# Optimization experiments

Measured on AMD Instinct MI355X. Metric: run time of the kernel, lower is better.

## Reference

```python
import jax, jax.numpy as jnp
import numpy as np

H = 768   # hidden_dim * SMPL_NR_JOINTS = 32 * 24
O = 72    # output_dim * SMPL_NR_JOINTS = 3 * 24
B = 256
T = 100   # max_len (tgt.size(1))
SRC_LEN = 16


def setup_inputs() -> dict:
    key = jax.random.key(0)
    ks = jax.random.split(key, 10)
    s = 1.0 / np.sqrt(H)
    return {
        "src": jax.random.normal(ks[0], (B, SRC_LEN, H), jnp.float32),
        "tgt": jax.random.normal(ks[1], (B, T, O), jnp.float32),
        "h0": jax.random.normal(ks[2], (B, H), jnp.float32),
        "c0": jax.random.normal(ks[3], (B, H), jnp.float32),
        "W_ih": jax.random.uniform(ks[4], (4 * H, H), jnp.float32, -s, s),
        "W_hh": jax.random.uniform(ks[5], (4 * H, H), jnp.float32, -s, s),
        "b_ih": jax.random.uniform(ks[6], (4 * H,), jnp.float32, -s, s),
        "b_hh": jax.random.uniform(ks[7], (4 * H,), jnp.float32, -s, s),
        "W_post": jax.random.uniform(ks[8], (O, H), jnp.float32, -s, s),
        "b_post": jax.random.uniform(ks[9], (O,), jnp.float32, -s, s),
    }


def reference(src, tgt, h0, c0, W_ih, W_hh, b_ih, b_hh, W_post, b_post):
    max_len = tgt.shape[1]
    bias = b_ih + b_hh  # [4H]

    def step(carry, _):
        x, h, c = carry  # each [B, H]
        gates = x @ W_ih.T + h @ W_hh.T + bias  # [B, 4H]
        i, f, g, o = jnp.split(gates, 4, axis=-1)  # PyTorch gate order i,f,g,o
        c = jax.nn.sigmoid(f) * c + jax.nn.sigmoid(i) * jnp.tanh(g)
        h = jax.nn.sigmoid(o) * jnp.tanh(c)
        return (h, h, c), h  # decoder output feeds back as next input

    x0 = src[:, -1]  # out = src[:, -1].unsqueeze(1)
    _, outs = jax.lax.scan(step, (x0, h0, c0), None, length=max_len)  # [T, B, H]
    outs = jnp.transpose(outs, (1, 0, 2))  # [B, T, H]
    return outs @ W_post.T + b_post  # [B, T, O]
```

## Files before the change

### kernel.cpp

```cpp
#include <hip/hip_runtime.h>
#include <hip/hip_bf16.h>
#include <math.h>

#define H 768
#define B 256
#define T 100

typedef __attribute__((ext_vector_type(8))) short short8;
typedef __attribute__((ext_vector_type(4))) float f32x4;
typedef unsigned long long u64;

static __device__ __forceinline__ float sigm(float x) {
    return 1.0f / (1.0f + __expf(-x));
}
static __device__ __forceinline__ float tanh_fast(float x) {
    return 1.0f - 2.0f / (__expf(2.0f * x) + 1.0f);
}

__global__ void prep_all(const float* __restrict__ src, const float* __restrict__ h0,
                         const float* __restrict__ Wih, const float* __restrict__ Whh,
                         const float* __restrict__ bih, const float* __restrict__ bhh,
                         const float* __restrict__ Wpost,
                         __hip_bfloat16* __restrict__ Wc,
                         __hip_bfloat16* __restrict__ Wcat,
                         float* __restrict__ bias,
                         __hip_bfloat16* __restrict__ Wp,
                         __hip_bfloat16* __restrict__ A0,
                         u64* __restrict__ sig64)
{
    const int bx = blockIdx.x;
    const int y  = blockIdx.y;
    const int k  = bx * 256 + threadIdx.x;
    if (y < 3072) {
        float a = Wih[y * H + k];
        float b = Whh[y * H + k];
        Wc[y * H + k] = __float2bfloat16(a + b);
        Wcat[y * 1536 + k] = __float2bfloat16(a);
        Wcat[y * 1536 + H + k] = __float2bfloat16(b);
        if (bx == 0 && threadIdx.x == 0) bias[y] = bih[y] + bhh[y];
    } else if (y < 3152) {
        int r = y - 3072;
        Wp[r * H + k] = (r < 72) ? __float2bfloat16(Wpost[r * H + k])
                                 : __float2bfloat16(0.0f);
    } else if (y < 3408) {
        int b = y - 3152;
        A0[b * 1536 + k] = __float2bfloat16(src[(b * 16 + 15) * H + k]);
        A0[b * 1536 + H + k] = __float2bfloat16(h0[b * H + k]);
    } else {
        sig64[(size_t)(y - 3408) * 768 + k] = 0ull;
    }
}

#define LDS_H_STRIDE  772
#define LDS_T0_STRIDE 1540
#define XCH_STRIDE    17

#define LDW8(n0,n1,n2,n3,n4,n5,n6,n7, p) \
    asm volatile("global_load_dwordx4 %0, %8, off\n\t" \
                 "global_load_dwordx4 %1, %8, off offset:64\n\t" \
                 "global_load_dwordx4 %2, %8, off offset:128\n\t" \
                 "global_load_dwordx4 %3, %8, off offset:192\n\t" \
                 "global_load_dwordx4 %4, %8, off offset:256\n\t" \
                 "global_load_dwordx4 %5, %8, off offset:320\n\t" \
                 "global_load_dwordx4 %6, %8, off offset:384\n\t" \
                 "global_load_dwordx4 %7, %8, off offset:448\n\t" \
                 "s_waitcnt vmcnt(0)" \
                 : "=&v"(n0),"=&v"(n1),"=&v"(n2),"=&v"(n3), \
                   "=&v"(n4),"=&v"(n5),"=&v"(n6),"=&v"(n7) \
                 : "v"(p))

#define KSTEP(nm, idx) { \
    short8 a_ = *(const short8*)(&lds_h[col * LDS_H_STRIDE + (idx) * 32 + quad * 8]); \
    acc = __builtin_amdgcn_mfma_f32_16x16x32_bf16(a_, nm, acc, 0, 0, 0); }

static __device__ __forceinline__ bool sig_ok(u64 x) {
    return (unsigned short)x && (unsigned short)(x >> 16) &&
           (unsigned short)(x >> 32) && (unsigned short)(x >> 48);
}

__global__ __launch_bounds__(768, 3) void lstm_persist(
    const __hip_bfloat16* __restrict__ Wc,
    const __hip_bfloat16* __restrict__ Wcat,
    const float* __restrict__ bias,
    const float* __restrict__ c0in,
    const __hip_bfloat16* __restrict__ A0,
    unsigned* sig)
{
    const int mtg  = blockIdx.x >> 4;
    const int jg   = blockIdx.x & 15;
    const int tid  = threadIdx.x;
    const int lane = tid & 63;
    const int wave = tid >> 6;
    const int col  = lane & 15;
    const int quad = lane >> 4;
    const int jt_l = wave >> 2;
    const int gate = wave & 3;
    const int j    = jg * 48 + jt_l * 16 + col;

    __shared__ short lds_h[16 * LDS_T0_STRIDE];
    __shared__ float xch[12 * 16 * XCH_STRIDE];

    const short* wptr = (const short*)Wc + (size_t)(gate * H + j) * H + quad * 8;
    short8 w00,w01,w02,w03,w04,w05,w06,w07,w08,w09,w10,w11,
           w12,w13,w14,w15,w16,w17,w18,w19,w20,w21,w22,w23;
    LDW8(w00,w01,w02,w03,w04,w05,w06,w07, wptr);
    LDW8(w08,w09,w10,w11,w12,w13,w14,w15, wptr + 256);
    LDW8(w16,w17,w18,w19,w20,w21,w22,w23, wptr + 512);

    const int p    = tid;
    const int bb   = p / 24;
    const int jp   = p % 24;
    const int jloc = jp * 2;
    const int cjt  = jloc >> 4;
    const int jcol = jloc & 15;
    const int bglob = mtg * 16 + bb;
    const int jglob = jg * 48 + jloc;
    float c0v = 0.f, c1v = 0.f;
    float bi0=0,bi1=0,bf0=0,bf1=0,bg0=0,bg1=0,bo0=0,bo1=0;
    if (p < 384) {
        c0v = c0in[(size_t)bglob * H + jglob];
        c1v = c0in[(size_t)bglob * H + jglob + 1];
        bi0 = bias[0*H + jglob]; bi1 = bias[0*H + jglob + 1];
        bf0 = bias[1*H + jglob]; bf1 = bias[1*H + jglob + 1];
        bg0 = bias[2*H + jglob]; bg1 = bias[2*H + jglob + 1];
        bo0 = bias[3*H + jglob]; bo1 = bias[3*H + jglob + 1];
    }

    const u64* sig64c = (const u64*)sig;
    const int r0  = tid / 192;
    const int wrd = tid % 192;

    for (int t = 0; t < T; ++t) {
        f32x4 acc = {0.f, 0.f, 0.f, 0.f};

        if (t == 0) {
            const u64* a8 = (const u64*)((const short*)A0 + (size_t)(mtg * 16) * 1536);
#pragma unroll
            for (int i = 0; i < 8; ++i) {
                int idx = tid + i * 768;
                int br  = idx / 384;
                int ch  = idx % 384;
                *(u64*)&lds_h[br * LDS_T0_STRIDE + ch * 4] = a8[(size_t)br * 384 + ch];
            }
            __syncthreads();

            const short* wq = (const short*)Wcat + (size_t)(gate * H + j) * 1536 + quad * 8;
            for (int kk = 0; kk < 48; ++kk) {
                short8 a_ = *(const short8*)(&lds_h[col * LDS_T0_STRIDE + kk * 32 + quad * 8]);
                short8 b_ = *(const short8*)(wq + kk * 32);
                acc = __builtin_amdgcn_mfma_f32_16x16x32_bf16(a_, b_, acc, 0, 0, 0);
            }
        } else {
            const u64* hb = sig64c + ((size_t)(t - 1) * B + (size_t)(mtg * 16)) * 192 + wrd;
            u64 x0 = __hip_atomic_load(hb + (size_t)(r0     ) * 192,
                                       __ATOMIC_RELAXED, __HIP_MEMORY_SCOPE_AGENT);
            u64 x1 = __hip_atomic_load(hb + (size_t)(r0 +  4) * 192,
                                       __ATOMIC_RELAXED, __HIP_MEMORY_SCOPE_AGENT);
            u64 x2 = __hip_atomic_load(hb + (size_t)(r0 +  8) * 192,
                                       __ATOMIC_RELAXED, __HIP_MEMORY_SCOPE_AGENT);
            u64 x3 = __hip_atomic_load(hb + (size_t)(r0 + 12) * 192,
                                       __ATOMIC_RELAXED, __HIP_MEMORY_SCOPE_AGENT);
            unsigned pending = 0xFu;
            if (sig_ok(x0)) { *(u64*)&lds_h[(r0     ) * LDS_H_STRIDE + wrd * 4] = ~x0; pending &= ~1u; }
            if (sig_ok(x1)) { *(u64*)&lds_h[(r0 +  4) * LDS_H_STRIDE + wrd * 4] = ~x1; pending &= ~2u; }
            if (sig_ok(x2)) { *(u64*)&lds_h[(r0 +  8) * LDS_H_STRIDE + wrd * 4] = ~x2; pending &= ~4u; }
            if (sig_ok(x3)) { *(u64*)&lds_h[(r0 + 12) * LDS_H_STRIDE + wrd * 4] = ~x3; pending &= ~8u; }
            int guard = 0;
            while (pending && ++guard < (1 << 22)) {
                __builtin_amdgcn_s_sleep(4);
                if (pending & 1u) x0 = __hip_atomic_load(hb + (size_t)(r0     ) * 192,
                                        __ATOMIC_RELAXED, __HIP_MEMORY_SCOPE_AGENT);
                if (pending & 2u) x1 = __hip_atomic_load(hb + (size_t)(r0 +  4) * 192,
                                        __ATOMIC_RELAXED, __HIP_MEMORY_SCOPE_AGENT);
                if (pending & 4u) x2 = __hip_atomic_load(hb + (size_t)(r0 +  8) * 192,
                                        __ATOMIC_RELAXED, __HIP_MEMORY_SCOPE_AGENT);
                if (pending & 8u) x3 = __hip_atomic_load(hb + (size_t)(r0 + 12) * 192,
                                        __ATOMIC_RELAXED, __HIP_MEMORY_SCOPE_AGENT);
                if ((pending & 1u) && sig_ok(x0)) { *(u64*)&lds_h[(r0     ) * LDS_H_STRIDE + wrd * 4] = ~x0; pending &= ~1u; }
                if ((pending & 2u) && sig_ok(x1)) { *(u64*)&lds_h[(r0 +  4) * LDS_H_STRIDE + wrd * 4] = ~x1; pending &= ~2u; }
                if ((pending & 4u) && sig_ok(x2)) { *(u64*)&lds_h[(r0 +  8) * LDS_H_STRIDE + wrd * 4] = ~x2; pending &= ~4u; }
                if ((pending & 8u) && sig_ok(x3)) { *(u64*)&lds_h[(r0 + 12) * LDS_H_STRIDE + wrd * 4] = ~x3; pending &= ~8u; }
            }
            __syncthreads();

            KSTEP(w00,0)  KSTEP(w01,1)  KSTEP(w02,2)  KSTEP(w03,3)
            KSTEP(w04,4)  KSTEP(w05,5)  KSTEP(w06,6)  KSTEP(w07,7)
            KSTEP(w08,8)  KSTEP(w09,9)  KSTEP(w10,10) KSTEP(w11,11)
            KSTEP(w12,12) KSTEP(w13,13) KSTEP(w14,14) KSTEP(w15,15)
            KSTEP(w16,16) KSTEP(w17,17) KSTEP(w18,18) KSTEP(w19,19)
            KSTEP(w20,20) KSTEP(w21,21) KSTEP(w22,22) KSTEP(w23,23)
        }

        float* xw = &xch[(size_t)wave * 16 * XCH_STRIDE];
#pragma unroll
        for (int r = 0; r < 4; ++r)
            xw[(quad * 4 + r) * XCH_STRIDE + col] = acc[r];
        __syncthreads();

        if (p < 384) {
            const float* xg = &xch[(size_t)(cjt * 4) * 16 * XCH_STRIDE + bb * XCH_STRIDE + jcol];
            const int gs = 16 * XCH_STRIDE;
            float i0 = xg[0*gs] + bi0, i1 = xg[0*gs + 1] + bi1;
            float f0 = xg[1*gs] + bf0, f1 = xg[1*gs + 1] + bf1;
            float g0 = xg[2*gs] + bg0, g1 = xg[2*gs + 1] + bg1;
            float o0 = xg[3*gs] + bo0, o1 = xg[3*gs + 1] + bo1;
            float cn0 = sigm(f0) * c0v + sigm(i0) * tanh_fast(g0);
            float cn1 = sigm(f1) * c1v + sigm(i1) * tanh_fast(g1);
            c0v = cn0; c1v = cn1;
            __hip_bfloat16 h0b = __float2bfloat16(sigm(o0) * tanh_fast(cn0));
            __hip_bfloat16 h1b = __float2bfloat16(sigm(o1) * tanh_fast(cn1));
            unsigned lo = (unsigned)(unsigned short)~(*(unsigned short*)&h0b);
            unsigned hi = (unsigned)(unsigned short)~(*(unsigned short*)&h1b);
            __hip_atomic_store(&sig[((size_t)t * B + bglob) * 384 + (jglob >> 1)],
                               lo | (hi << 16),
                               __ATOMIC_RELAXED, __HIP_MEMORY_SCOPE_AGENT);
        }
        __syncthreads();
    }
}

__global__ __launch_bounds__(64) void proj(
    const short* __restrict__ Hs,
    const __hip_bfloat16* __restrict__ Wp,
    const float* __restrict__ bpost,
    float* __restrict__ out)
{
    const int mt = blockIdx.x;
    const int lane = threadIdx.x;
    const int col = lane & 15;
    const int quad = lane >> 4;

    const short* Ap = Hs + (size_t)(mt * 16 + col) * H + quad * 8;
    const short* Wb = (const short*)Wp;

    f32x4 acc[5];
#pragma unroll
    for (int nt = 0; nt < 5; ++nt) acc[nt] = (f32x4){0.f, 0.f, 0.f, 0.f};

    for (int k = 0; k < H; k += 32) {
        short8 a = ~(*(const short8*)(Ap + k));
#pragma unroll
        for (int nt = 0; nt < 5; ++nt) {
            short8 b = *(const short8*)(Wb + (size_t)(nt * 16 + col) * H + quad * 8 + k);
            acc[nt] = __builtin_amdgcn_mfma_f32_16x16x32_bf16(a, b, acc[nt], 0, 0, 0);
        }
    }

#pragma unroll
    for (int nt = 0; nt < 5; ++nt) {
        const int o = nt * 16 + col;
        if (o < 72) {
            const float bb = bpost[o];
#pragma unroll
            for (int r = 0; r < 4; ++r) {
                const int m = mt * 16 + quad * 4 + r;
                const int t = m >> 8;
                const int b = m & 255;
                out[((size_t)b * T + t) * 72 + o] = acc[nt][r] + bb;
            }
        }
    }
}


extern "C" void kernel_launch(void* const* d_in, const int* in_sizes, int n_in,
                              void* d_out, int out_size, void* d_ws, size_t ws_size,
                              hipStream_t stream) {
    const float* src   = (const float*)d_in[0];
    const float* h0    = (const float*)d_in[2];
    const float* c0    = (const float*)d_in[3];
    const float* Wih   = (const float*)d_in[4];
    const float* Whh   = (const float*)d_in[5];
    const float* bih   = (const float*)d_in[6];
    const float* bhh   = (const float*)d_in[7];
    const float* Wpost = (const float*)d_in[8];
    const float* bpost = (const float*)d_in[9];
    float* out = (float*)d_out;

    char* ws = (char*)d_ws;
    __hip_bfloat16* Wcat = (__hip_bfloat16*)(ws + 0);
    __hip_bfloat16* Wc   = (__hip_bfloat16*)(ws + 9437184);
    float*          bias = (float*)(ws + 14155776);
    __hip_bfloat16* Wp   = (__hip_bfloat16*)(ws + 14168064);
    __hip_bfloat16* A0   = (__hip_bfloat16*)(ws + 14290944);
    unsigned*       sig  = (unsigned*)(ws + 15863808);

    prep_all<<<dim3(3, 9808), 256, 0, stream>>>(src, h0, Wih, Whh, bih, bhh, Wpost,
                                                Wc, Wcat, bias, Wp, A0, (u64*)sig);

    lstm_persist<<<256, 768, 0, stream>>>(Wc, Wcat, bias, c0, A0, sig);

    proj<<<1600, 64, 0, stream>>>((const short*)sig, Wp, bpost, out);
}
```

Baseline: 460.5 us.

## Remap persistent LSTM blocks by XCD and poll with non-coherent sc0 loads

At kernel start each block reads its hardware XCD id and takes a slot from a per-XCD counter. When every XCD holds exactly 32 blocks, it remaps (batch tile, hidden group) so each batch tile's 16 hidden groups sit on one XCD, keeping h-state exchange inside a shared L2. The h-state polling now first uses sc0 loads with shorter sleeps and falls back to agent-scope atomic loads after a few sweeps. This is meant to cut cross-XCD coherence latency in the per-timestep handoff. It adds a startup grid-wide barrier, and it relies on all 256 blocks being co-resident and on sc0 loads observing other blocks' writes within the same XCD.

```diff
diff --git a/kernel.cpp b/kernel.cpp
--- a/kernel.cpp
+++ b/kernel.cpp
@@ -26,7 +26,8 @@
                          float* __restrict__ bias,
                          __hip_bfloat16* __restrict__ Wp,
                          __hip_bfloat16* __restrict__ A0,
-                         u64* __restrict__ sig64)
+                         u64* __restrict__ sig64,
+                         unsigned* __restrict__ ctrl)
 {
     const int bx = blockIdx.x;
     const int y  = blockIdx.y;
@@ -48,12 +49,15 @@
         A0[b * 1536 + H + k] = __float2bfloat16(h0[b * H + k]);
     } else {
         sig64[(size_t)(y - 3408) * 768 + k] = 0ull;
+        if (y == 3408 && bx == 0 && threadIdx.x < 16) ctrl[threadIdx.x] = 0u;
     }
 }
 
 #define LDS_H_STRIDE  772
 #define LDS_T0_STRIDE 1540
 #define XCH_STRIDE    17
+#define GUARD_MAX     (1 << 22)
+#define ESC_SWEEPS    4
 
 #define LDW8(n0,n1,n2,n3,n4,n5,n6,n7, p) \
     asm volatile("global_load_dwordx4 %0, %8, off\n\t" \
@@ -69,6 +73,24 @@
                    "=&v"(n4),"=&v"(n5),"=&v"(n6),"=&v"(n7) \
                  : "v"(p))
 
+#define LDP4_SC0(x0,x1,x2,x3, p0,p1,p2,p3) \
+    asm volatile("global_load_dwordx2 %0, %4, off sc0\n\t" \
+                 "global_load_dwordx2 %1, %5, off sc0\n\t" \
+                 "global_load_dwordx2 %2, %6, off sc0\n\t" \
+                 "global_load_dwordx2 %3, %7, off sc0\n\t" \
+                 "s_waitcnt vmcnt(0)" \
+                 : "=&v"(x0),"=&v"(x1),"=&v"(x2),"=&v"(x3) \
+                 : "v"(p0),"v"(p1),"v"(p2),"v"(p3))
+
+#define AG_LD(p) __hip_atomic_load((p), __ATOMIC_RELAXED, __HIP_MEMORY_SCOPE_AGENT)
+
+static __device__ __forceinline__ u64 ld2_sc0(const u64* p) {
+    u64 r;
+    asm volatile("global_load_dwordx2 %0, %1, off sc0\n\ts_waitcnt vmcnt(0)"
+                 : "=v"(r) : "v"(p));
+    return r;
+}
+
 #define KSTEP(nm, idx) { \
     short8 a_ = *(const short8*)(&lds_h[col * LDS_H_STRIDE + (idx) * 32 + quad * 8]); \
     acc = __builtin_amdgcn_mfma_f32_16x16x32_bf16(a_, nm, acc, 0, 0, 0); }
@@ -84,10 +106,9 @@
     const float* __restrict__ bias,
     const float* __restrict__ c0in,
     const __hip_bfloat16* __restrict__ A0,
-    unsigned* sig)
+    unsigned* sig,
+    unsigned* ctrl)
 {
-    const int mtg  = blockIdx.x >> 4;
-    const int jg   = blockIdx.x & 15;
     const int tid  = threadIdx.x;
     const int lane = tid & 63;
     const int wave = tid >> 6;
@@ -95,10 +116,39 @@
     const int quad = lane >> 4;
     const int jt_l = wave >> 2;
     const int gate = wave & 3;
-    const int j    = jg * 48 + jt_l * 16 + col;
 
     __shared__ short lds_h[16 * LDS_T0_STRIDE];
     __shared__ float xch[12 * 16 * XCH_STRIDE];
+    __shared__ unsigned s_role[2];
+
+    if (tid == 0) {
+        unsigned xcd;
+        asm volatile("s_getreg_b32 %0, hwreg(HW_REG_XCC_ID)" : "=s"(xcd));
+        xcd &= 7u;
+        unsigned slot = __hip_atomic_fetch_add(&ctrl[xcd], 1u,
+                            __ATOMIC_RELAXED, __HIP_MEMORY_SCOPE_AGENT);
+        if (slot >= 32u)
+            __hip_atomic_store(&ctrl[9], 1u, __ATOMIC_RELEASE, __HIP_MEMORY_SCOPE_AGENT);
+        __hip_atomic_fetch_add(&ctrl[8], 1u, __ATOMIC_RELEASE, __HIP_MEMORY_SCOPE_AGENT);
+        int cg = 0;
+        while (__hip_atomic_load(&ctrl[8], __ATOMIC_ACQUIRE, __HIP_MEMORY_SCOPE_AGENT) < 256u
+               && ++cg < GUARD_MAX)
+            __builtin_amdgcn_s_sleep(8);
+        s_role[0] = xcd * 32u + slot;
+        s_role[1] = __hip_atomic_load(&ctrl[9], __ATOMIC_ACQUIRE, __HIP_MEMORY_SCOPE_AGENT);
+    }
+    __syncthreads();
+    const bool LOCAL = (s_role[1] == 0u);
+    int mtg, jg;
+    if (LOCAL) {
+        const unsigned slot32 = s_role[0] & 31u;
+        mtg = (int)((s_role[0] >> 5) * 2u + (slot32 >> 4));
+        jg  = (int)(slot32 & 15u);
+    } else {
+        mtg = blockIdx.x >> 4;
+        jg  = blockIdx.x & 15;
+    }
+    const int j = jg * 48 + jt_l * 16 + col;
 
     const short* wptr = (const short*)Wc + (size_t)(gate * H + j) * H + quad * 8;
     short8 w00,w01,w02,w03,w04,w05,w06,w07,w08,w09,w10,w11,
@@ -152,34 +202,30 @@
             }
         } else {
             const u64* hb = sig64c + ((size_t)(t - 1) * B + (size_t)(mtg * 16)) * 192 + wrd;
-            u64 x0 = __hip_atomic_load(hb + (size_t)(r0     ) * 192,
-                                       __ATOMIC_RELAXED, __HIP_MEMORY_SCOPE_AGENT);
-            u64 x1 = __hip_atomic_load(hb + (size_t)(r0 +  4) * 192,
-                                       __ATOMIC_RELAXED, __HIP_MEMORY_SCOPE_AGENT);
-            u64 x2 = __hip_atomic_load(hb + (size_t)(r0 +  8) * 192,
-                                       __ATOMIC_RELAXED, __HIP_MEMORY_SCOPE_AGENT);
-            u64 x3 = __hip_atomic_load(hb + (size_t)(r0 + 12) * 192,
-                                       __ATOMIC_RELAXED, __HIP_MEMORY_SCOPE_AGENT);
+            const u64* q0 = hb + (size_t)(r0     ) * 192;
+            const u64* q1 = hb + (size_t)(r0 +  4) * 192;
+            const u64* q2 = hb + (size_t)(r0 +  8) * 192;
+            const u64* q3 = hb + (size_t)(r0 + 12) * 192;
+            u64 x0, x1, x2, x3;
+            LDP4_SC0(x0, x1, x2, x3, q0, q1, q2, q3);
             unsigned pending = 0xFu;
             if (sig_ok(x0)) { *(u64*)&lds_h[(r0     ) * LDS_H_STRIDE + wrd * 4] = ~x0; pending &= ~1u; }
             if (sig_ok(x1)) { *(u64*)&lds_h[(r0 +  4) * LDS_H_STRIDE + wrd * 4] = ~x1; pending &= ~2u; }
             if (sig_ok(x2)) { *(u64*)&lds_h[(r0 +  8) * LDS_H_STRIDE + wrd * 4] = ~x2; pending &= ~4u; }
             if (sig_ok(x3)) { *(u64*)&lds_h[(r0 + 12) * LDS_H_STRIDE + wrd * 4] = ~x3; pending &= ~8u; }
             int guard = 0;
-            while (pending && ++guard < (1 << 22)) {
-                __builtin_amdgcn_s_sleep(4);
-                if (pending & 1u) x0 = __hip_atomic_load(hb + (size_t)(r0     ) * 192,
-                                        __ATOMIC_RELAXED, __HIP_MEMORY_SCOPE_AGENT);
-                if (pending & 2u) x1 = __hip_atomic_load(hb + (size_t)(r0 +  4) * 192,
-                                        __ATOMIC_RELAXED, __HIP_MEMORY_SCOPE_AGENT);
-                if (pending & 4u) x2 = __hip_atomic_load(hb + (size_t)(r0 +  8) * 192,
-                                        __ATOMIC_RELAXED, __HIP_MEMORY_SCOPE_AGENT);
-                if (pending & 8u) x3 = __hip_atomic_load(hb + (size_t)(r0 + 12) * 192,
-                                        __ATOMIC_RELAXED, __HIP_MEMORY_SCOPE_AGENT);
-                if ((pending & 1u) && sig_ok(x0)) { *(u64*)&lds_h[(r0     ) * LDS_H_STRIDE + wrd * 4] = ~x0; pending &= ~1u; }
-                if ((pending & 2u) && sig_ok(x1)) { *(u64*)&lds_h[(r0 +  4) * LDS_H_STRIDE + wrd * 4] = ~x1; pending &= ~2u; }
-                if ((pending & 4u) && sig_ok(x2)) { *(u64*)&lds_h[(r0 +  8) * LDS_H_STRIDE + wrd * 4] = ~x2; pending &= ~4u; }
-                if ((pending & 8u) && sig_ok(x3)) { *(u64*)&lds_h[(r0 + 12) * LDS_H_STRIDE + wrd * 4] = ~x3; pending &= ~8u; }
+            while (pending && ++guard < GUARD_MAX) {
+                if (guard < ESC_SWEEPS) __builtin_amdgcn_s_sleep(2);
+                else                    __builtin_amdgcn_s_sleep(4);
+                const bool esc = (guard >= ESC_SWEEPS);
+                if (pending & 1u) { x0 = esc ? AG_LD(q0) : ld2_sc0(q0);
+                    if (sig_ok(x0)) { *(u64*)&lds_h[(r0     ) * LDS_H_STRIDE + wrd * 4] = ~x0; pending &= ~1u; } }
+                if (pending & 2u) { x1 = esc ? AG_LD(q1) : ld2_sc0(q1);
+                    if (sig_ok(x1)) { *(u64*)&lds_h[(r0 +  4) * LDS_H_STRIDE + wrd * 4] = ~x1; pending &= ~2u; } }
+                if (pending & 4u) { x2 = esc ? AG_LD(q2) : ld2_sc0(q2);
+                    if (sig_ok(x2)) { *(u64*)&lds_h[(r0 +  8) * LDS_H_STRIDE + wrd * 4] = ~x2; pending &= ~4u; } }
+                if (pending & 8u) { x3 = esc ? AG_LD(q3) : ld2_sc0(q3);
+                    if (sig_ok(x3)) { *(u64*)&lds_h[(r0 + 12) * LDS_H_STRIDE + wrd * 4] = ~x3; pending &= ~8u; } }
             }
             __syncthreads();
 
@@ -283,12 +329,13 @@
     float*          bias = (float*)(ws + 14155776);
     __hip_bfloat16* Wp   = (__hip_bfloat16*)(ws + 14168064);
     __hip_bfloat16* A0   = (__hip_bfloat16*)(ws + 14290944);
+    unsigned*       ctrl = (unsigned*)(ws + 15077376);
     unsigned*       sig  = (unsigned*)(ws + 15863808);
 
     prep_all<<<dim3(3, 9808), 256, 0, stream>>>(src, h0, Wih, Whh, bih, bhh, Wpost,
-                                                Wc, Wcat, bias, Wp, A0, (u64*)sig);
-
-    lstm_persist<<<256, 768, 0, stream>>>(Wc, Wcat, bias, c0, A0, sig);
+                                                Wc, Wcat, bias, Wp, A0, (u64*)sig, ctrl);
+
+    lstm_persist<<<256, 768, 0, stream>>>(Wc, Wcat, bias, c0, A0, sig, ctrl);
 
     proj<<<1600, 64, 0, stream>>>((const short*)sig, Wp, bpost, out);
 }
```

After: 737.0 us. 1.6x slower.

## Add per-block step counters to gate polling before reading hidden-state signals

Applied to the files above, without the earlier changes.

Adds a per-block flag array that each block bumps with a release store after finishing a timestep. Before loading the previous step's hidden state, 16 threads spin on the 16 producer flags for their batch group, then all threads read the data once with sc1 vector loads. This replaces all 768 threads repeatedly polling the self-validating payload words, aiming to cut memory traffic and contention during the cross-block exchange. The cost is an extra flag round trip, a block barrier and a full vmcnt wait on every step, which could add latency on the critical path.

```diff
diff --git a/kernel.cpp b/kernel.cpp
--- a/kernel.cpp
+++ b/kernel.cpp
@@ -26,7 +26,8 @@
                          float* __restrict__ bias,
                          __hip_bfloat16* __restrict__ Wp,
                          __hip_bfloat16* __restrict__ A0,
-                         u64* __restrict__ sig64)
+                         u64* __restrict__ sig64,
+                         unsigned* __restrict__ flags)
 {
     const int bx = blockIdx.x;
     const int y  = blockIdx.y;
@@ -48,12 +49,14 @@
         A0[b * 1536 + H + k] = __float2bfloat16(h0[b * H + k]);
     } else {
         sig64[(size_t)(y - 3408) * 768 + k] = 0ull;
+        if (y == 3408 && bx == 0) flags[threadIdx.x] = 0u;
     }
 }
 
 #define LDS_H_STRIDE  772
 #define LDS_T0_STRIDE 1540
 #define XCH_STRIDE    17
+#define GUARD_MAX     (1 << 22)
 
 #define LDW8(n0,n1,n2,n3,n4,n5,n6,n7, p) \
     asm volatile("global_load_dwordx4 %0, %8, off\n\t" \
@@ -69,6 +72,17 @@
                    "=&v"(n4),"=&v"(n5),"=&v"(n6),"=&v"(n7) \
                  : "v"(p))
 
+#define LDP4_AG(x0,x1,x2,x3, p0,p1,p2,p3) \
+    asm volatile("global_load_dwordx2 %0, %4, off sc1\n\t" \
+                 "global_load_dwordx2 %1, %5, off sc1\n\t" \
+                 "global_load_dwordx2 %2, %6, off sc1\n\t" \
+                 "global_load_dwordx2 %3, %7, off sc1\n\t" \
+                 "s_waitcnt vmcnt(0)" \
+                 : "=&v"(x0),"=&v"(x1),"=&v"(x2),"=&v"(x3) \
+                 : "v"(p0),"v"(p1),"v"(p2),"v"(p3))
+
+#define AG_LD(p) __hip_atomic_load((p), __ATOMIC_RELAXED, __HIP_MEMORY_SCOPE_AGENT)
+
 #define KSTEP(nm, idx) { \
     short8 a_ = *(const short8*)(&lds_h[col * LDS_H_STRIDE + (idx) * 32 + quad * 8]); \
     acc = __builtin_amdgcn_mfma_f32_16x16x32_bf16(a_, nm, acc, 0, 0, 0); }
@@ -84,7 +98,8 @@
     const float* __restrict__ bias,
     const float* __restrict__ c0in,
     const __hip_bfloat16* __restrict__ A0,
-    unsigned* sig)
+    unsigned* sig,
+    unsigned* flags)
 {
     const int mtg  = blockIdx.x >> 4;
     const int jg   = blockIdx.x & 15;
@@ -151,35 +166,40 @@
                 acc = __builtin_amdgcn_mfma_f32_16x16x32_bf16(a_, b_, acc, 0, 0, 0);
             }
         } else {
+            if (tid < 16) {
+                const unsigned tgt = (unsigned)t;
+                unsigned v = AG_LD(&flags[mtg * 16 + tid]);
+                int fg = 0;
+                while (v < tgt && ++fg < GUARD_MAX) {
+                    __builtin_amdgcn_s_sleep(1);
+                    v = AG_LD(&flags[mtg * 16 + tid]);
+                }
+            }
+            __syncthreads();
+
             const u64* hb = sig64c + ((size_t)(t - 1) * B + (size_t)(mtg * 16)) * 192 + wrd;
-            u64 x0 = __hip_atomic_load(hb + (size_t)(r0     ) * 192,
-                                       __ATOMIC_RELAXED, __HIP_MEMORY_SCOPE_AGENT);
-            u64 x1 = __hip_atomic_load(hb + (size_t)(r0 +  4) * 192,
-                                       __ATOMIC_RELAXED, __HIP_MEMORY_SCOPE_AGENT);
-            u64 x2 = __hip_atomic_load(hb + (size_t)(r0 +  8) * 192,
-                                       __ATOMIC_RELAXED, __HIP_MEMORY_SCOPE_AGENT);
-            u64 x3 = __hip_atomic_load(hb + (size_t)(r0 + 12) * 192,
-                                       __ATOMIC_RELAXED, __HIP_MEMORY_SCOPE_AGENT);
+            const u64* q0 = hb + (size_t)(r0     ) * 192;
+            const u64* q1 = hb + (size_t)(r0 +  4) * 192;
+            const u64* q2 = hb + (size_t)(r0 +  8) * 192;
+            const u64* q3 = hb + (size_t)(r0 + 12) * 192;
+            u64 x0, x1, x2, x3;
+            LDP4_AG(x0, x1, x2, x3, q0, q1, q2, q3);
             unsigned pending = 0xFu;
             if (sig_ok(x0)) { *(u64*)&lds_h[(r0     ) * LDS_H_STRIDE + wrd * 4] = ~x0; pending &= ~1u; }
             if (sig_ok(x1)) { *(u64*)&lds_h[(r0 +  4) * LDS_H_STRIDE + wrd * 4] = ~x1; pending &= ~2u; }
             if (sig_ok(x2)) { *(u64*)&lds_h[(r0 +  8) * LDS_H_STRIDE + wrd * 4] = ~x2; pending &= ~4u; }
             if (sig_ok(x3)) { *(u64*)&lds_h[(r0 + 12) * LDS_H_STRIDE + wrd * 4] = ~x3; pending &= ~8u; }
             int guard = 0;
-            while (pending && ++guard < (1 << 22)) {
+            while (pending && ++guard < GUARD_MAX) {
                 __builtin_amdgcn_s_sleep(4);
-                if (pending & 1u) x0 = __hip_atomic_load(hb + (size_t)(r0     ) * 192,
-                                        __ATOMIC_RELAXED, __HIP_MEMORY_SCOPE_AGENT);
-                if (pending & 2u) x1 = __hip_atomic_load(hb + (size_t)(r0 +  4) * 192,
-                                        __ATOMIC_RELAXED, __HIP_MEMORY_SCOPE_AGENT);
-                if (pending & 4u) x2 = __hip_atomic_load(hb + (size_t)(r0 +  8) * 192,
-                                        __ATOMIC_RELAXED, __HIP_MEMORY_SCOPE_AGENT);
-                if (pending & 8u) x3 = __hip_atomic_load(hb + (size_t)(r0 + 12) * 192,
-                                        __ATOMIC_RELAXED, __HIP_MEMORY_SCOPE_AGENT);
-                if ((pending & 1u) && sig_ok(x0)) { *(u64*)&lds_h[(r0     ) * LDS_H_STRIDE + wrd * 4] = ~x0; pending &= ~1u; }
-                if ((pending & 2u) && sig_ok(x1)) { *(u64*)&lds_h[(r0 +  4) * LDS_H_STRIDE + wrd * 4] = ~x1; pending &= ~2u; }
-                if ((pending & 4u) && sig_ok(x2)) { *(u64*)&lds_h[(r0 +  8) * LDS_H_STRIDE + wrd * 4] = ~x2; pending &= ~4u; }
-                if ((pending & 8u) && sig_ok(x3)) { *(u64*)&lds_h[(r0 + 12) * LDS_H_STRIDE + wrd * 4] = ~x3; pending &= ~8u; }
+                if (pending & 1u) { x0 = AG_LD(q0);
+                    if (sig_ok(x0)) { *(u64*)&lds_h[(r0     ) * LDS_H_STRIDE + wrd * 4] = ~x0; pending &= ~1u; } }
+                if (pending & 2u) { x1 = AG_LD(q1);
+                    if (sig_ok(x1)) { *(u64*)&lds_h[(r0 +  4) * LDS_H_STRIDE + wrd * 4] = ~x1; pending &= ~2u; } }
+                if (pending & 4u) { x2 = AG_LD(q2);
+                    if (sig_ok(x2)) { *(u64*)&lds_h[(r0 +  8) * LDS_H_STRIDE + wrd * 4] = ~x2; pending &= ~4u; } }
+                if (pending & 8u) { x3 = AG_LD(q3);
+                    if (sig_ok(x3)) { *(u64*)&lds_h[(r0 + 12) * LDS_H_STRIDE + wrd * 4] = ~x3; pending &= ~8u; } }
             }
             __syncthreads();
 
@@ -215,7 +235,12 @@
                                lo | (hi << 16),
                                __ATOMIC_RELAXED, __HIP_MEMORY_SCOPE_AGENT);
         }
+        asm volatile("s_waitcnt vmcnt(0)" ::: "memory");
         __syncthreads();
+
+        if (tid == 0)
+            __hip_atomic_store(&flags[mtg * 16 + jg], (unsigned)(t + 1),
+                               __ATOMIC_RELEASE, __HIP_MEMORY_SCOPE_AGENT);
     }
 }
 
@@ -283,12 +308,13 @@
     float*          bias = (float*)(ws + 14155776);
     __hip_bfloat16* Wp   = (__hip_bfloat16*)(ws + 14168064);
     __hip_bfloat16* A0   = (__hip_bfloat16*)(ws + 14290944);
+    unsigned*       flags= (unsigned*)(ws + 15077376);
     unsigned*       sig  = (unsigned*)(ws + 15863808);
 
     prep_all<<<dim3(3, 9808), 256, 0, stream>>>(src, h0, Wih, Whh, bih, bhh, Wpost,
-                                                Wc, Wcat, bias, Wp, A0, (u64*)sig);
-
-    lstm_persist<<<256, 768, 0, stream>>>(Wc, Wcat, bias, c0, A0, sig);
+                                                Wc, Wcat, bias, Wp, A0, (u64*)sig, flags);
+
+    lstm_persist<<<256, 768, 0, stream>>>(Wc, Wcat, bias, c0, A0, sig, flags);
 
     proj<<<1600, 64, 0, stream>>>((const short*)sig, Wp, bpost, out);
 }
```

Result: slower. 899.9 us (+95.4%).

## Fuse output projection into persistent LSTM kernel tail

Applied to the files above, without the earlier changes.

Removes the separate projection kernel and computes the output projection at the end of the persistent LSTM kernel. Each wave handles one timestep for its batch tile, reading stored h from the signal buffer with sc1 loads, and the final timestep is first waited for and staged into LDS. This saves a kernel launch and lets the projection run on blocks already resident. In exchange the projection uses only 100 waves per batch group, with uneven load across blocks, and it relies on the spin-wait for the last step's h.

```diff
diff --git a/kernel.cpp b/kernel.cpp
--- a/kernel.cpp
+++ b/kernel.cpp
@@ -69,6 +69,17 @@
                    "=&v"(n4),"=&v"(n5),"=&v"(n6),"=&v"(n7) \
                  : "v"(p))
 
+#define LDA6(n0,n1,n2,n3,n4,n5, p) \
+    asm volatile("global_load_dwordx4 %0, %6, off sc1\n\t" \
+                 "global_load_dwordx4 %1, %6, off offset:64 sc1\n\t" \
+                 "global_load_dwordx4 %2, %6, off offset:128 sc1\n\t" \
+                 "global_load_dwordx4 %3, %6, off offset:192 sc1\n\t" \
+                 "global_load_dwordx4 %4, %6, off offset:256 sc1\n\t" \
+                 "global_load_dwordx4 %5, %6, off offset:320 sc1\n\t" \
+                 "s_waitcnt vmcnt(0)" \
+                 : "=&v"(n0),"=&v"(n1),"=&v"(n2),"=&v"(n3),"=&v"(n4),"=&v"(n5) \
+                 : "v"(p))
+
 #define KSTEP(nm, idx) { \
     short8 a_ = *(const short8*)(&lds_h[col * LDS_H_STRIDE + (idx) * 32 + quad * 8]); \
     acc = __builtin_amdgcn_mfma_f32_16x16x32_bf16(a_, nm, acc, 0, 0, 0); }
@@ -84,7 +95,10 @@
     const float* __restrict__ bias,
     const float* __restrict__ c0in,
     const __hip_bfloat16* __restrict__ A0,
-    unsigned* sig)
+    unsigned* sig,
+    const __hip_bfloat16* __restrict__ Wp,
+    const float* __restrict__ bpost,
+    float* __restrict__ out)
 {
     const int mtg  = blockIdx.x >> 4;
     const int jg   = blockIdx.x & 15;
@@ -217,46 +231,90 @@
         }
         __syncthreads();
     }
-}
-
-__global__ __launch_bounds__(64) void proj(
-    const short* __restrict__ Hs,
-    const __hip_bfloat16* __restrict__ Wp,
-    const float* __restrict__ bpost,
-    float* __restrict__ out)
-{
-    const int mt = blockIdx.x;
-    const int lane = threadIdx.x;
-    const int col = lane & 15;
-    const int quad = lane >> 4;
-
-    const short* Ap = Hs + (size_t)(mt * 16 + col) * H + quad * 8;
-    const short* Wb = (const short*)Wp;
-
-    f32x4 acc[5];
-#pragma unroll
-    for (int nt = 0; nt < 5; ++nt) acc[nt] = (f32x4){0.f, 0.f, 0.f, 0.f};
-
-    for (int k = 0; k < H; k += 32) {
-        short8 a = ~(*(const short8*)(Ap + k));
-#pragma unroll
-        for (int nt = 0; nt < 5; ++nt) {
-            short8 b = *(const short8*)(Wb + (size_t)(nt * 16 + col) * H + quad * 8 + k);
-            acc[nt] = __builtin_amdgcn_mfma_f32_16x16x32_bf16(a, b, acc[nt], 0, 0, 0);
+
+    {
+        const u64* hb = sig64c + ((size_t)(T - 1) * B + (size_t)(mtg * 16)) * 192 + wrd;
+        u64 x0 = __hip_atomic_load(hb + (size_t)(r0     ) * 192,
+                                   __ATOMIC_RELAXED, __HIP_MEMORY_SCOPE_AGENT);
+        u64 x1 = __hip_atomic_load(hb + (size_t)(r0 +  4) * 192,
+                                   __ATOMIC_RELAXED, __HIP_MEMORY_SCOPE_AGENT);
+        u64 x2 = __hip_atomic_load(hb + (size_t)(r0 +  8) * 192,
+                                   __ATOMIC_RELAXED, __HIP_MEMORY_SCOPE_AGENT);
+        u64 x3 = __hip_atomic_load(hb + (size_t)(r0 + 12) * 192,
+                                   __ATOMIC_RELAXED, __HIP_MEMORY_SCOPE_AGENT);
+        unsigned pending = 0xFu;
+        if (sig_ok(x0)) { *(u64*)&lds_h[(r0     ) * LDS_H_STRIDE + wrd * 4] = ~x0; pending &= ~1u; }
+        if (sig_ok(x1)) { *(u64*)&lds_h[(r0 +  4) * LDS_H_STRIDE + wrd * 4] = ~x1; pending &= ~2u; }
+        if (sig_ok(x2)) { *(u64*)&lds_h[(r0 +  8) * LDS_H_STRIDE + wrd * 4] = ~x2; pending &= ~4u; }
+        if (sig_ok(x3)) { *(u64*)&lds_h[(r0 + 12) * LDS_H_STRIDE + wrd * 4] = ~x3; pending &= ~8u; }
+        int guard = 0;
+        while (pending && ++guard < (1 << 22)) {
+            __builtin_amdgcn_s_sleep(4);
+            if (pending & 1u) { x0 = __hip_atomic_load(hb + (size_t)(r0     ) * 192,
+                                    __ATOMIC_RELAXED, __HIP_MEMORY_SCOPE_AGENT);
+                if (sig_ok(x0)) { *(u64*)&lds_h[(r0     ) * LDS_H_STRIDE + wrd * 4] = ~x0; pending &= ~1u; } }
+            if (pending & 2u) { x1 = __hip_atomic_load(hb + (size_t)(r0 +  4) * 192,
+                                    __ATOMIC_RELAXED, __HIP_MEMORY_SCOPE_AGENT);
+                if (sig_ok(x1)) { *(u64*)&lds_h[(r0 +  4) * LDS_H_STRIDE + wrd * 4] = ~x1; pending &= ~2u; } }
+            if (pending & 4u) { x2 = __hip_atomic_load(hb + (size_t)(r0 +  8) * 192,
+                                    __ATOMIC_RELAXED, __HIP_MEMORY_SCOPE_AGENT);
+                if (sig_ok(x2)) { *(u64*)&lds_h[(r0 +  8) * LDS_H_STRIDE + wrd * 4] = ~x2; pending &= ~4u; } }
+            if (pending & 8u) { x3 = __hip_atomic_load(hb + (size_t)(r0 + 12) * 192,
+                                    __ATOMIC_RELAXED, __HIP_MEMORY_SCOPE_AGENT);
+                if (sig_ok(x3)) { *(u64*)&lds_h[(r0 + 12) * LDS_H_STRIDE + wrd * 4] = ~x3; pending &= ~8u; } }
         }
-    }
-
-#pragma unroll
-    for (int nt = 0; nt < 5; ++nt) {
-        const int o = nt * 16 + col;
-        if (o < 72) {
-            const float bb = bpost[o];
-#pragma unroll
-            for (int r = 0; r < 4; ++r) {
-                const int m = mt * 16 + quad * 4 + r;
-                const int t = m >> 8;
-                const int b = m & 255;
-                out[((size_t)b * T + t) * 72 + o] = acc[nt][r] + bb;
+        __syncthreads();
+    }
+
+    {
+        const int wv = jg * 12 + wave;
+        if (wv < T) {
+            const int t = wv;
+            const short* Wb = (const short*)Wp;
+            f32x4 pacc[5];
+#pragma unroll
+            for (int nt = 0; nt < 5; ++nt) pacc[nt] = (f32x4){0.f, 0.f, 0.f, 0.f};
+
+            if (t == T - 1) {
+                for (int kk = 0; kk < 24; ++kk) {
+                    short8 a = *(const short8*)(&lds_h[col * LDS_H_STRIDE + kk * 32 + quad * 8]);
+#pragma unroll
+                    for (int nt = 0; nt < 5; ++nt) {
+                        short8 b = *(const short8*)(Wb + (size_t)(nt * 16 + col) * H + quad * 8 + kk * 32);
+                        pacc[nt] = __builtin_amdgcn_mfma_f32_16x16x32_bf16(a, b, pacc[nt], 0, 0, 0);
+                    }
+                }
+            } else {
+                const short* Ap = (const short*)sig + ((size_t)t * B + (size_t)(mtg * 16 + col)) * H + quad * 8;
+#pragma unroll
+                for (int g6 = 0; g6 < 4; ++g6) {
+                    short8 a0, a1, a2, a3, a4, a5;
+                    LDA6(a0, a1, a2, a3, a4, a5, Ap + g6 * 192);
+                    const short* wk = Wb + (size_t)quad * 8 + (size_t)g6 * 192;
+#pragma unroll
+                    for (int nt = 0; nt < 5; ++nt) {
+                        const short* wr = wk + (size_t)(nt * 16 + col) * H;
+                        pacc[nt] = __builtin_amdgcn_mfma_f32_16x16x32_bf16(~a0, *(const short8*)(wr      ), pacc[nt], 0, 0, 0);
+                        pacc[nt] = __builtin_amdgcn_mfma_f32_16x16x32_bf16(~a1, *(const short8*)(wr +  32), pacc[nt], 0, 0, 0);
+                        pacc[nt] = __builtin_amdgcn_mfma_f32_16x16x32_bf16(~a2, *(const short8*)(wr +  64), pacc[nt], 0, 0, 0);
+                        pacc[nt] = __builtin_amdgcn_mfma_f32_16x16x32_bf16(~a3, *(const short8*)(wr +  96), pacc[nt], 0, 0, 0);
+                        pacc[nt] = __builtin_amdgcn_mfma_f32_16x16x32_bf16(~a4, *(const short8*)(wr + 128), pacc[nt], 0, 0, 0);
+                        pacc[nt] = __builtin_amdgcn_mfma_f32_16x16x32_bf16(~a5, *(const short8*)(wr + 160), pacc[nt], 0, 0, 0);
+                    }
+                }
+            }
+
+#pragma unroll
+            for (int nt = 0; nt < 5; ++nt) {
+                const int o = nt * 16 + col;
+                if (o < 72) {
+                    const float bb2 = bpost[o];
+#pragma unroll
+                    for (int r = 0; r < 4; ++r) {
+                        const int b = mtg * 16 + quad * 4 + r;
+                        out[((size_t)b * T + t) * 72 + o] = pacc[nt][r] + bb2;
+                    }
+                }
             }
         }
     }
@@ -288,7 +346,6 @@
     prep_all<<<dim3(3, 9808), 256, 0, stream>>>(src, h0, Wih, Whh, bih, bhh, Wpost,
                                                 Wc, Wcat, bias, Wp, A0, (u64*)sig);
 
-    lstm_persist<<<256, 768, 0, stream>>>(Wc, Wcat, bias, c0, A0, sig);
-
-    proj<<<1600, 64, 0, stream>>>((const short*)sig, Wp, bpost, out);
-}
+    lstm_persist<<<256, 768, 0, stream>>>(Wc, Wcat, bias, c0, A0, sig,
+                                          Wp, bpost, out);
+}
```

Result: slower. 492.9 us (+7.0%).
